# Performance work log

Hardware: AMD Instinct MI355X
Metric: run time of the kernel (lower is better)

The kernel has to match this reference:

```python
import jax, jax.numpy as jnp
import numpy as np

B, T, E, HID, K = 64, 512, 768, 256, 11
H = HID // 2  # per-direction LSTM hidden = 128


def setup_inputs() -> dict:
    key = jax.random.key(0)
    ks = iter(jax.random.split(key, 40))

    def gn(shape, s=0.08):
        return jax.random.normal(next(ks), shape, jnp.float32) * s

    inp = {}
    inp["embeds"] = jax.random.normal(next(ks), (B, T, E), jnp.float32)
    inp["tags"] = jax.random.randint(next(ks), (B, T), 0, K)
    inp["mask"] = jnp.ones((B, T), jnp.bool_)
    # 2-layer bidirectional LSTM params, PyTorch layout: W_ih [4H, din], gate order i,f,g,o
    for l, din in ((0, E), (1, HID)):
        for sfx in ("", "_r"):
            inp[f"w_ih_l{l}{sfx}"] = gn((4 * H, din))
            inp[f"w_hh_l{l}{sfx}"] = gn((4 * H, H))
            inp[f"b_ih_l{l}{sfx}"] = gn((4 * H,))
            inp[f"b_hh_l{l}{sfx}"] = gn((4 * H,))
    inp["linear_w"] = gn((K, HID))
    inp["linear_b"] = gn((K,))
    inp["start_trans"] = gn((K,))
    inp["end_trans"] = gn((K,))
    inp["trans"] = gn((K, K))
    return inp


def _lstm_dir(xs, wih, whh, bih, bhh, reverse):
    # xs: [T, B, din] -> [T, B, H]; PyTorch gate order i, f, g, o
    Hn = whh.shape[1]
    h0 = jnp.zeros((xs.shape[1], Hn), xs.dtype)

    def step(carry, xt):
        h, c = carry
        g = xt @ wih.T + h @ whh.T + bih + bhh
        i, f, gg, o = jnp.split(g, 4, axis=-1)
        c = jax.nn.sigmoid(f) * c + jax.nn.sigmoid(i) * jnp.tanh(gg)
        h = jax.nn.sigmoid(o) * jnp.tanh(c)
        return (h, c), h

    _, hs = jax.lax.scan(step, (h0, h0), xs, reverse=reverse)
    return hs


def reference(embeds, tags, mask,
              w_ih_l0, w_hh_l0, b_ih_l0, b_hh_l0,
              w_ih_l0_r, w_hh_l0_r, b_ih_l0_r, b_hh_l0_r,
              w_ih_l1, w_hh_l1, b_ih_l1, b_hh_l1,
              w_ih_l1_r, w_hh_l1_r, b_ih_l1_r, b_hh_l1_r,
              linear_w, linear_b, start_trans, end_trans, trans):
    xs = jnp.transpose(embeds, (1, 0, 2))  # [T, B, E]
    # BiLSTM layer 0 and 1 (dropout p=0.1 is identity in eval/deterministic reference)
    h0 = jnp.concatenate([
        _lstm_dir(xs, w_ih_l0, w_hh_l0, b_ih_l0, b_hh_l0, False),
        _lstm_dir(xs, w_ih_l0_r, w_hh_l0_r, b_ih_l0_r, b_hh_l0_r, True)], axis=-1)
    h1 = jnp.concatenate([
        _lstm_dir(h0, w_ih_l1, w_hh_l1, b_ih_l1, b_hh_l1, False),
        _lstm_dir(h0, w_ih_l1_r, w_hh_l1_r, b_ih_l1_r, b_hh_l1_r, True)], axis=-1)
    em = h1 @ linear_w.T + linear_b  # emissions [T, B, K]

    tags_t = tags.T                    # [T, B]
    mask_f = mask.T.astype(em.dtype)   # [T, B]
    bidx = jnp.arange(em.shape[1])

    # ---- CRF numerator (gold path score), torchcrf semantics ----
    num = start_trans[tags_t[0]] + em[0, bidx, tags_t[0]]
    trans_sc = trans[tags_t[:-1], tags_t[1:]]                                   # [T-1, B]
    emit_sc = jnp.take_along_axis(em[1:], tags_t[1:, :, None], axis=2)[..., 0]  # [T-1, B]
    num = num + jnp.sum((trans_sc + emit_sc) * mask_f[1:], axis=0)
    seq_ends = jnp.sum(mask.astype(jnp.int32), axis=1) - 1
    num = num + end_trans[tags[bidx, seq_ends]]

    # ---- CRF denominator (log partition, forward algorithm as one scan) ----
    def fstep(score, xt):
        em_t, m_t = xt
        nxt = jax.nn.logsumexp(score[:, :, None] + trans[None] + em_t[:, None, :], axis=1)
        return jnp.where(m_t[:, None] > 0, nxt, score), None

    score, _ = jax.lax.scan(fstep, start_trans[None] + em[0], (em[1:], mask_f[1:]))
    den = jax.nn.logsumexp(score + end_trans[None], axis=1)

    # loss = -crf(emissions, tags, mask, reduction='mean')
    return -jnp.mean(num - den)
```

## Files before the change

kernel.cpp:

```cpp
#include <hip/hip_runtime.h>
#include <hip/hip_bf16.h>

typedef unsigned short u16;
typedef __bf16 bf16x8 __attribute__((ext_vector_type(8)));
typedef float f32x4 __attribute__((ext_vector_type(4)));
typedef u16 u16x8 __attribute__((ext_vector_type(8)));

__device__ __forceinline__ float bf2f(u16 u) {
    unsigned x = ((unsigned)u) << 16;
    return __builtin_bit_cast(float, x);
}
__device__ __forceinline__ u16 f2bf(float f) {
    unsigned x = __builtin_bit_cast(unsigned, f);
    unsigned r = (x + 0x7fffu + ((x >> 16) & 1u)) >> 16;
    return (u16)r;
}
__device__ __forceinline__ float sigm(float x) { return 1.f / (1.f + __expf(-x)); }
__device__ __forceinline__ float tanh_fast(float x) { return 1.f - 2.f / (1.f + __expf(2.f * x)); }

__global__ void convw_kernel(const float* __restrict__ wf, const float* __restrict__ wr,
                             u16* __restrict__ out, int half_rows, int K) {
    int idx = blockIdx.x * 256 + threadIdx.x;
    int total = 2 * half_rows * K;
    if (idx >= total) return;
    int n = idx / K, k = idx - n * K;
    float v = (n < half_rows) ? wf[(size_t)n * K + k] : wr[(size_t)(n - half_rows) * K + k];
    out[idx] = f2bf(v);
}

template <bool AF32>
__global__ __launch_bounds__(256, 2) void gemm_bf16_bt(const void* __restrict__ Av,
                                                       const u16* __restrict__ B,
                                                       u16* __restrict__ C,
                                                       int M, int N, int K) {
    __shared__ __align__(16) u16 As[128 * 40];
    __shared__ __align__(16) u16 Bs[128 * 40];
    const int tid = threadIdx.x;
    const int n0 = blockIdx.x * 128, m0 = blockIdx.y * 128;
    const int srow = tid >> 1, shalf = tid & 1;
    const int lane = tid & 63, wv = tid >> 6;
    const int wm = wv >> 1, wn = wv & 1;
    const int frow = lane & 15, fko = (lane >> 4) * 8;
    f32x4 acc[4][4] = {};
    const int nk = K >> 5;
    for (int kt = 0; kt < nk; ++kt) {
        u16x8 a0, a1;
        if (AF32) {
            const float* ap = (const float*)Av + (size_t)(m0 + srow) * K + kt * 32 + shalf * 16;
            f32x4 f0 = *(const f32x4*)(ap);
            f32x4 f1 = *(const f32x4*)(ap + 4);
            f32x4 f2 = *(const f32x4*)(ap + 8);
            f32x4 f3 = *(const f32x4*)(ap + 12);
#pragma unroll
            for (int x = 0; x < 4; x++) {
                a0[x] = f2bf(f0[x]); a0[4 + x] = f2bf(f1[x]);
                a1[x] = f2bf(f2[x]); a1[4 + x] = f2bf(f3[x]);
            }
        } else {
            const u16* ap = (const u16*)Av + (size_t)(m0 + srow) * K + kt * 32 + shalf * 16;
            a0 = *(const u16x8*)(ap);
            a1 = *(const u16x8*)(ap + 8);
        }
        const u16* bp = B + (size_t)(n0 + srow) * K + kt * 32 + shalf * 16;
        u16x8 b0 = *(const u16x8*)(bp);
        u16x8 b1 = *(const u16x8*)(bp + 8);
        __syncthreads();
        *(u16x8*)&As[srow * 40 + shalf * 16] = a0;
        *(u16x8*)&As[srow * 40 + shalf * 16 + 8] = a1;
        *(u16x8*)&Bs[srow * 40 + shalf * 16] = b0;
        *(u16x8*)&Bs[srow * 40 + shalf * 16 + 8] = b1;
        __syncthreads();
        bf16x8 af[4], bfr[4];
#pragma unroll
        for (int mi = 0; mi < 4; mi++)
            af[mi] = *(const bf16x8*)&As[(wm * 64 + mi * 16 + frow) * 40 + fko];
#pragma unroll
        for (int ni = 0; ni < 4; ni++)
            bfr[ni] = *(const bf16x8*)&Bs[(wn * 64 + ni * 16 + frow) * 40 + fko];
#pragma unroll
        for (int mi = 0; mi < 4; mi++)
#pragma unroll
            for (int ni = 0; ni < 4; ni++)
                acc[mi][ni] = __builtin_amdgcn_mfma_f32_16x16x32_bf16(af[mi], bfr[ni], acc[mi][ni], 0, 0, 0);
    }
#pragma unroll
    for (int mi = 0; mi < 4; mi++)
#pragma unroll
        for (int ni = 0; ni < 4; ni++)
#pragma unroll
            for (int r = 0; r < 4; r++) {
                int row = m0 + wm * 64 + mi * 16 + (lane >> 4) * 4 + r;
                int col = n0 + wn * 64 + ni * 16 + (lane & 15);
                C[(size_t)row * N + col] = f2bf(acc[mi][ni][r]);
            }
}

__global__ __launch_bounds__(512, 2) void lstm_kernel(const u16* __restrict__ xproj,
                                                      const float* __restrict__ whh_f,
                                                      const float* __restrict__ whh_r,
                                                      const float* __restrict__ bih_f,
                                                      const float* __restrict__ bhh_f,
                                                      const float* __restrict__ bih_r,
                                                      const float* __restrict__ bhh_r,
                                                      u16* __restrict__ hout) {
    const int b = blockIdx.x, d = blockIdx.y;
    const int g = threadIdx.x;
    const float* whh = d ? whh_r : whh_f;
    f32x4 w[32];
    const f32x4* wrow = (const f32x4*)(whh + (size_t)g * 128);
#pragma unroll
    for (int i = 0; i < 32; i++) w[i] = wrow[i];
    float bsum = (d ? bih_r[g] : bih_f[g]) + (d ? bhh_r[g] : bhh_f[g]);
    __shared__ __align__(16) float h_lds[128];
    __shared__ float glds[512];
    if (g < 128) h_lds[g] = 0.f;
    float c = 0.f;
    __syncthreads();
    const u16* xp = xproj + (size_t)b * 512 * 1024 + (size_t)d * 512 + g;
    for (int s = 0; s < 512; ++s) {
        const int tt = d ? (511 - s) : s;
        float gbase = bsum + bf2f(xp[(size_t)tt * 1024]);
        float a0 = 0.f, a1 = 0.f, a2 = 0.f, a3 = 0.f;
        const f32x4* h4 = (const f32x4*)h_lds;
#pragma unroll
        for (int i = 0; i < 32; i++) {
            f32x4 hv = h4[i];
            a0 = fmaf(w[i][0], hv[0], a0);
            a1 = fmaf(w[i][1], hv[1], a1);
            a2 = fmaf(w[i][2], hv[2], a2);
            a3 = fmaf(w[i][3], hv[3], a3);
        }
        glds[g] = gbase + ((a0 + a1) + (a2 + a3));
        __syncthreads();
        if (g < 128) {
            float gi = glds[g], gf = glds[g + 128], gg = glds[g + 256], go = glds[g + 384];
            c = sigm(gf) * c + sigm(gi) * tanh_fast(gg);
            float h = sigm(go) * tanh_fast(c);
            h_lds[g] = h;
            hout[((size_t)b * 512 + tt) * 256 + (size_t)d * 128 + g] = f2bf(h);
        }
        __syncthreads();
    }
}

__global__ __launch_bounds__(256) void em_kernel(const u16* __restrict__ h1,
                                                 const float* __restrict__ lw,
                                                 const float* __restrict__ lb,
                                                 float* __restrict__ em) {
    __shared__ float w[11 * 256];
    for (int i = threadIdx.x; i < 11 * 256; i += 256) w[i] = lw[i];
    __syncthreads();
    int r = blockIdx.x * 256 + threadIdx.x;
    const u16x8* hp = (const u16x8*)(h1 + (size_t)r * 256);
    float acc[11];
#pragma unroll
    for (int j = 0; j < 11; j++) acc[j] = lb[j];
    for (int kc = 0; kc < 32; ++kc) {
        u16x8 hv = hp[kc];
        float hf[8];
#pragma unroll
        for (int x = 0; x < 8; x++) hf[x] = bf2f(hv[x]);
#pragma unroll
        for (int x = 0; x < 8; x++)
#pragma unroll
            for (int j = 0; j < 11; j++) acc[j] = fmaf(hf[x], w[j * 256 + kc * 8 + x], acc[j]);
    }
    int b = r >> 9, t = r & 511;
    float* o = em + ((size_t)t * 64 + b) * 16;
#pragma unroll
    for (int j = 0; j < 11; j++) o[j] = acc[j];
}

__global__ __launch_bounds__(64) void crf_kernel(const float* __restrict__ em,
                                                 const int* __restrict__ tags,
                                                 const float* __restrict__ start_trans,
                                                 const float* __restrict__ end_trans,
                                                 const float* __restrict__ trans,
                                                 float* __restrict__ pb) {
    const int lane = threadIdx.x;
    const int seg = lane >> 4, kp = lane & 15;
    const int kpc = kp < 11 ? kp : 10;
    const int b = blockIdx.x * 4 + seg;
    const int* tg = tags + (size_t)b * 512;
    float num = 0.f;
    for (int t = kp; t < 512; t += 16) {
        int cur = tg[t];
        float e = em[((size_t)t * 64 + b) * 16 + cur];
        float tr = (t == 0) ? start_trans[cur] : trans[tg[t - 1] * 11 + cur];
        num += e + tr;
    }
#pragma unroll
    for (int off = 8; off >= 1; off >>= 1) num += __shfl_down(num, off, 16);
    float trcol[11];
#pragma unroll
    for (int k = 0; k < 11; k++) trcol[k] = trans[k * 11 + kpc];
    float s = start_trans[kpc] + em[(size_t)b * 16 + kpc];
    for (int t = 1; t < 512; ++t) {
        float v[11], m = -1e30f;
#pragma unroll
        for (int k = 0; k < 11; k++) {
            v[k] = __shfl(s, k, 16) + trcol[k];
            m = fmaxf(m, v[k]);
        }
        float sum = 0.f;
#pragma unroll
        for (int k = 0; k < 11; k++) sum += __expf(v[k] - m);
        s = m + __logf(sum) + em[((size_t)t * 64 + b) * 16 + kpc];
    }
    float u = s + end_trans[kpc];
    float m2 = -1e30f, vv[11];
#pragma unroll
    for (int k = 0; k < 11; k++) {
        vv[k] = __shfl(u, k, 16);
        m2 = fmaxf(m2, vv[k]);
    }
    float s2 = 0.f;
#pragma unroll
    for (int k = 0; k < 11; k++) s2 += __expf(vv[k] - m2);
    float den = m2 + __logf(s2);
    if (kp == 0) {
        float numt = num + end_trans[tg[511]];
        pb[b] = numt - den;
    }
}

__global__ __launch_bounds__(64) void final_kernel(const float* __restrict__ pb, float* __restrict__ out) {
    float v = pb[threadIdx.x];
#pragma unroll
    for (int off = 32; off >= 1; off >>= 1) v += __shfl_down(v, off, 64);
    if (threadIdx.x == 0) out[0] = -(v / 64.f);
}

extern "C" void kernel_launch(void* const* d_in, const int* in_sizes, int n_in,
                              void* d_out, int out_size, void* d_ws, size_t ws_size,
                              hipStream_t stream) {
    const float* embeds = (const float*)d_in[0];
    const int* tags = (const int*)d_in[1];
    const float* wih0f = (const float*)d_in[3];
    const float* whh0f = (const float*)d_in[4];
    const float* bih0f = (const float*)d_in[5];
    const float* bhh0f = (const float*)d_in[6];
    const float* wih0r = (const float*)d_in[7];
    const float* whh0r = (const float*)d_in[8];
    const float* bih0r = (const float*)d_in[9];
    const float* bhh0r = (const float*)d_in[10];
    const float* wih1f = (const float*)d_in[11];
    const float* whh1f = (const float*)d_in[12];
    const float* bih1f = (const float*)d_in[13];
    const float* bhh1f = (const float*)d_in[14];
    const float* wih1r = (const float*)d_in[15];
    const float* whh1r = (const float*)d_in[16];
    const float* bih1r = (const float*)d_in[17];
    const float* bhh1r = (const float*)d_in[18];
    const float* lw = (const float*)d_in[19];
    const float* lb = (const float*)d_in[20];
    const float* st = (const float*)d_in[21];
    const float* et = (const float*)d_in[22];
    const float* tr = (const float*)d_in[23];
    float* out = (float*)d_out;

    char* ws = (char*)d_ws;
    u16* xproj = (u16*)(ws + 0);
    u16* h0 = (u16*)(ws + 67108864);
    u16* h1 = (u16*)(ws + 83886080);
    float* em = (float*)(ws + 100663296);
    u16* w0c = (u16*)(ws + 102760448);
    u16* w1c = (u16*)(ws + 104333312);
    float* pb = (float*)(ws + 104857600);

    convw_kernel<<<3072, 256, 0, stream>>>(wih0f, wih0r, w0c, 512, 768);
    convw_kernel<<<1024, 256, 0, stream>>>(wih1f, wih1r, w1c, 512, 256);
    gemm_bf16_bt<true><<<dim3(8, 256), 256, 0, stream>>>(embeds, w0c, xproj, 32768, 1024, 768);
    lstm_kernel<<<dim3(64, 2), 512, 0, stream>>>(xproj, whh0f, whh0r, bih0f, bhh0f, bih0r, bhh0r, h0);
    gemm_bf16_bt<false><<<dim3(8, 256), 256, 0, stream>>>(h0, w1c, xproj, 32768, 1024, 256);
    lstm_kernel<<<dim3(64, 2), 512, 0, stream>>>(xproj, whh1f, whh1r, bih1f, bhh1f, bih1r, bhh1r, h1);
    em_kernel<<<128, 256, 0, stream>>>(h1, lw, lb, em);
    crf_kernel<<<16, 64, 0, stream>>>(em, tags, st, et, tr, pb);
    final_kernel<<<1, 64, 0, stream>>>(pb, out);
}
```

Baseline: 1.354 ms.

## Use MFMA for LSTM recurrence with two sequences per block and double-buffered h

Replaces the scalar-FMA recurrent matvec with bf16 MFMA. The W_hh fragments are kept in registers, each block processes two batch sequences, and the hidden state is double-buffered in LDS, so each timestep needs one barrier instead of two. The next step's input projection is prefetched while the current gates are computed, and sigmoid/tanh use the hardware reciprocal. The gate math is fused into every thread, which removes the separate gate-exchange pass. This trades fp32 precision of W_hh and h for bf16, and only 64 blocks are launched.

```diff
diff --git a/kernel.cpp b/kernel.cpp
--- a/kernel.cpp
+++ b/kernel.cpp
@@ -15,8 +15,12 @@
     unsigned r = (x + 0x7fffu + ((x >> 16) & 1u)) >> 16;
     return (u16)r;
 }
-__device__ __forceinline__ float sigm(float x) { return 1.f / (1.f + __expf(-x)); }
-__device__ __forceinline__ float tanh_fast(float x) { return 1.f - 2.f / (1.f + __expf(2.f * x)); }
+__device__ __forceinline__ float sigm(float x) {
+    return __builtin_amdgcn_rcpf(1.f + __expf(-x));
+}
+__device__ __forceinline__ float tanh_fast(float x) {
+    return 1.f - 2.f * __builtin_amdgcn_rcpf(1.f + __expf(2.f * x));
+}
 
 __global__ void convw_kernel(const float* __restrict__ wf, const float* __restrict__ wr,
                              u16* __restrict__ out, int half_rows, int K) {
@@ -95,51 +99,99 @@
             }
 }
 
-__global__ __launch_bounds__(512, 2) void lstm_kernel(const u16* __restrict__ xproj,
-                                                      const float* __restrict__ whh_f,
-                                                      const float* __restrict__ whh_r,
-                                                      const float* __restrict__ bih_f,
-                                                      const float* __restrict__ bhh_f,
-                                                      const float* __restrict__ bih_r,
-                                                      const float* __restrict__ bhh_r,
-                                                      u16* __restrict__ hout) {
-    const int b = blockIdx.x, d = blockIdx.y;
-    const int g = threadIdx.x;
+__global__ __launch_bounds__(256, 1) void lstm_mfma(const u16* __restrict__ xproj,
+                                                    const float* __restrict__ whh_f,
+                                                    const float* __restrict__ whh_r,
+                                                    const float* __restrict__ bih_f,
+                                                    const float* __restrict__ bhh_f,
+                                                    const float* __restrict__ bih_r,
+                                                    const float* __restrict__ bhh_r,
+                                                    u16* __restrict__ hout) {
+    const int p = blockIdx.x;
+    const int d = blockIdx.y;
+    const int tid = threadIdx.x;
+    const int w = tid >> 6, l = tid & 63;
     const float* whh = d ? whh_r : whh_f;
-    f32x4 w[32];
-    const f32x4* wrow = (const f32x4*)(whh + (size_t)g * 128);
-#pragma unroll
-    for (int i = 0; i < 32; i++) w[i] = wrow[i];
-    float bsum = (d ? bih_r[g] : bih_f[g]) + (d ? bhh_r[g] : bhh_f[g]);
-    __shared__ __align__(16) float h_lds[128];
-    __shared__ float glds[512];
-    if (g < 128) h_lds[g] = 0.f;
-    float c = 0.f;
+    const float* bih = d ? bih_r : bih_f;
+    const float* bhh = d ? bhh_r : bhh_f;
+
+    bf16x8 bf[8][4];
+#pragma unroll
+    for (int k = 0; k < 8; ++k) {
+        const float* wr = whh + (size_t)((w + 4 * k) * 16 + (l & 15)) * 128;
+#pragma unroll
+        for (int c = 0; c < 4; ++c) {
+            f32x4 x0 = *(const f32x4*)(wr + c * 32 + (l >> 4) * 8);
+            f32x4 x1 = *(const f32x4*)(wr + c * 32 + (l >> 4) * 8 + 4);
+            u16x8 t;
+#pragma unroll
+            for (int x = 0; x < 4; x++) { t[x] = f2bf(x0[x]); t[4 + x] = f2bf(x1[x]); }
+            bf[k][c] = __builtin_bit_cast(bf16x8, t);
+        }
+    }
+
+    const int jcol = l & 15, jg = (l >> 4) & 1, b = l >> 5;
+    const int j = jg * 64 + w * 16 + jcol;
+    float bias[4];
+#pragma unroll
+    for (int gt = 0; gt < 4; gt++) bias[gt] = bih[gt * 128 + j] + bhh[gt * 128 + j];
+
+    __shared__ __align__(16) u16 h_lds[2][16 * 136];
+    for (int i = tid; i < 2 * 16 * 136; i += 256) ((u16*)h_lds)[i] = 0;
+
+    const u16* xb = xproj + (size_t)(2 * p + b) * 512 * 1024 + (size_t)d * 512 + j;
+    u16 xv[4];
+    {
+        const int tt0 = d ? 511 : 0;
+#pragma unroll
+        for (int gt = 0; gt < 4; gt++) xv[gt] = xb[(size_t)tt0 * 1024 + gt * 128];
+    }
+    float c_state = 0.f;
+    u16* ho = hout + (size_t)(2 * p + b) * 512 * 256 + (size_t)d * 128 + j;
+    int cur = 0;
     __syncthreads();
-    const u16* xp = xproj + (size_t)b * 512 * 1024 + (size_t)d * 512 + g;
+
     for (int s = 0; s < 512; ++s) {
         const int tt = d ? (511 - s) : s;
-        float gbase = bsum + bf2f(xp[(size_t)tt * 1024]);
-        float a0 = 0.f, a1 = 0.f, a2 = 0.f, a3 = 0.f;
-        const f32x4* h4 = (const f32x4*)h_lds;
-#pragma unroll
-        for (int i = 0; i < 32; i++) {
-            f32x4 hv = h4[i];
-            a0 = fmaf(w[i][0], hv[0], a0);
-            a1 = fmaf(w[i][1], hv[1], a1);
-            a2 = fmaf(w[i][2], hv[2], a2);
-            a3 = fmaf(w[i][3], hv[3], a3);
-        }
-        glds[g] = gbase + ((a0 + a1) + (a2 + a3));
+        bf16x8 af[4];
+#pragma unroll
+        for (int c = 0; c < 4; ++c)
+            af[c] = *(const bf16x8*)&h_lds[cur][(l & 15) * 136 + c * 32 + (l >> 4) * 8];
+        f32x4 acc[8];
+#pragma unroll
+        for (int k = 0; k < 8; ++k)
+            acc[k] = __builtin_amdgcn_mfma_f32_16x16x32_bf16(af[0], bf[k][0], (f32x4){0.f, 0.f, 0.f, 0.f}, 0, 0, 0);
+#pragma unroll
+        for (int c = 1; c < 4; ++c)
+#pragma unroll
+            for (int k = 0; k < 8; ++k)
+                acc[k] = __builtin_amdgcn_mfma_f32_16x16x32_bf16(af[c], bf[k][c], acc[k], 0, 0, 0);
+        float gval[4];
+#pragma unroll
+        for (int gt = 0; gt < 4; gt++) {
+            float x00 = __shfl(acc[2 * gt][0], jcol, 64);
+            float x10 = __shfl(acc[2 * gt + 1][0], jcol, 64);
+            float x01 = __shfl(acc[2 * gt][1], jcol, 64);
+            float x11 = __shfl(acc[2 * gt + 1][1], jcol, 64);
+            float xa = jg ? x10 : x00;
+            float xc = jg ? x11 : x01;
+            gval[gt] = (b ? xc : xa) + bf2f(xv[gt]) + bias[gt];
+        }
+        {
+            const int s2 = (s + 1) & 511;
+            const int tt2 = d ? (511 - s2) : s2;
+#pragma unroll
+            for (int gt = 0; gt < 4; gt++) xv[gt] = xb[(size_t)tt2 * 1024 + gt * 128];
+        }
+        float ip = sigm(gval[0]), fp = sigm(gval[1]);
+        float tg = tanh_fast(gval[2]), op = sigm(gval[3]);
+        c_state = fp * c_state + ip * tg;
+        float h = op * tanh_fast(c_state);
+        u16 hb = f2bf(h);
+        h_lds[cur ^ 1][b * 136 + j] = hb;
+        ho[(size_t)tt * 256] = hb;
         __syncthreads();
-        if (g < 128) {
-            float gi = glds[g], gf = glds[g + 128], gg = glds[g + 256], go = glds[g + 384];
-            c = sigm(gf) * c + sigm(gi) * tanh_fast(gg);
-            float h = sigm(go) * tanh_fast(c);
-            h_lds[g] = h;
-            hout[((size_t)b * 512 + tt) * 256 + (size_t)d * 128 + g] = f2bf(h);
-        }
-        __syncthreads();
+        cur ^= 1;
     }
 }
 
@@ -271,9 +323,9 @@
     convw_kernel<<<3072, 256, 0, stream>>>(wih0f, wih0r, w0c, 512, 768);
     convw_kernel<<<1024, 256, 0, stream>>>(wih1f, wih1r, w1c, 512, 256);
     gemm_bf16_bt<true><<<dim3(8, 256), 256, 0, stream>>>(embeds, w0c, xproj, 32768, 1024, 768);
-    lstm_kernel<<<dim3(64, 2), 512, 0, stream>>>(xproj, whh0f, whh0r, bih0f, bhh0f, bih0r, bhh0r, h0);
+    lstm_mfma<<<dim3(32, 2), 256, 0, stream>>>(xproj, whh0f, whh0r, bih0f, bhh0f, bih0r, bhh0r, h0);
     gemm_bf16_bt<false><<<dim3(8, 256), 256, 0, stream>>>(h0, w1c, xproj, 32768, 1024, 256);
-    lstm_kernel<<<dim3(64, 2), 512, 0, stream>>>(xproj, whh1f, whh1r, bih1f, bhh1f, bih1r, bhh1r, h1);
+    lstm_mfma<<<dim3(32, 2), 256, 0, stream>>>(xproj, whh1f, whh1r, bih1f, bhh1f, bih1r, bhh1r, h1);
     em_kernel<<<128, 256, 0, stream>>>(h1, lw, lb, em);
     crf_kernel<<<16, 64, 0, stream>>>(em, tags, st, et, tr, pb);
     final_kernel<<<1, 64, 0, stream>>>(pb, out);
```

Result: faster. 1.239 ms (-8.5%).
